# Kernel optimization log

Hardware: AMD Instinct MI355X
Metric: run time of the kernel (lower is better)

The kernel has to match this reference:

```python
import jax, jax.numpy as jnp
import numpy as np

M_TIME = 64      # signal model output length (time points)
N_DICT = 20000   # dictionary entries
B_VOX = 8192     # voxels / batch


def setup_inputs() -> dict:
    key = jax.random.key(0)
    k = jax.random.split(key, 6)
    input_real = jax.random.normal(k[0], (M_TIME, B_VOX), jnp.float32)
    input_imag = jax.random.normal(k[1], (M_TIME, B_VOX), jnp.float32)
    # raw dictionary signals, then normalize columns as append() does
    yr = jax.random.normal(k[2], (M_TIME, N_DICT), jnp.float32)
    yi = jax.random.normal(k[3], (M_TIME, N_DICT), jnp.float32)
    norm = jnp.sqrt(jnp.sum(yr * yr + yi * yi, axis=0))  # (N,)
    inverse_norm_y = 1.0 / norm
    y_real = yr * inverse_norm_y
    y_imag = yi * inverse_norm_y
    x_t1 = jax.random.uniform(k[4], (N_DICT,), jnp.float32, 0.1, 3.0)
    x_t2 = jax.random.uniform(k[5], (N_DICT,), jnp.float32, 0.01, 0.5)
    return {
        'input_real': input_real, 'input_imag': input_imag,
        'y_real': y_real, 'y_imag': y_imag,
        'inverse_norm_y': inverse_norm_y, 'x_t1': x_t1, 'x_t2': x_t2,
    }


def reference(input_real, input_imag, y_real, y_imag, inverse_norm_y, x_t1, x_t2):
    # |<y_n, s_b>|^2 for complex y and complex input, via 4 real GEMMs (as in the
    # original module): sim[n, b]
    sim = (jnp.einsum('mb,mn->nb', input_real, y_real) ** 2
           + jnp.einsum('mb,mn->nb', input_real, y_imag) ** 2
           + jnp.einsum('mb,mn->nb', input_imag, y_real) ** 2
           + jnp.einsum('mb,mn->nb', input_imag, y_imag) ** 2)
    idx = jnp.argmax(sim, axis=0)  # (B,)
    # scale = sum_m conj(y[:, idx]) * input * inverse_norm_y[idx]
    yr = y_real[:, idx]   # (M, B)
    yi = y_imag[:, idx]   # (M, B)
    inv = inverse_norm_y[idx]  # (B,)
    scale_r = jnp.sum(yr * input_real + yi * input_imag, axis=0) * inv
    scale_i = jnp.sum(yr * input_imag - yi * input_real, axis=0) * inv
    # returns (scale, t1, t2) with complex scale split into real/imag, stacked (4, B)
    return jnp.stack([scale_r, scale_i, x_t1[idx], x_t2[idx]])
```

## Files before the change

### kernel.cpp

```cpp
#include <hip/hip_runtime.h>
#include <hip/hip_bf16.h>
#include <stdint.h>

#define M_TIME 64
#define N_DICT 20000
#define B_VOX  8192

#define NTILES 313

typedef _Float16 v8h __attribute__((ext_vector_type(8)));
typedef _Float16 v4h __attribute__((ext_vector_type(4)));
typedef float    v4f __attribute__((ext_vector_type(4)));
typedef __attribute__((address_space(3))) unsigned int  lds_u32;
typedef const __attribute__((address_space(1))) unsigned int glb_u32;

__device__ __forceinline__ unsigned long long u64max(unsigned long long a, unsigned long long b) { return a > b ? a : b; }
__device__ __forceinline__ unsigned umin32(unsigned a, unsigned b) { return a < b ? a : b; }
__device__ __forceinline__ unsigned umax32(unsigned a, unsigned b) { return a > b ? a : b; }

__global__ __launch_bounds__(256) void split_y(
    const float* __restrict__ yr, const float* __restrict__ yi,
    v4h* __restrict__ yp)
{
    const int u = blockIdx.x * 256 + threadIdx.x;
    const int n_l = u & 63;
    const int kq  = (u >> 6) & 15;
    const int T   = (u >> 10) % NTILES;
    const int arr = u / (NTILES * 1024);
    if (arr > 1) return;
    const float* P = arr ? yi : yr;
    const int n_g = T * 64 + n_l;
    float v0 = 0.f, v1 = 0.f, v2 = 0.f, v3 = 0.f;
    if (n_g < N_DICT) {
        v0 = P[(kq * 4 + 0) * N_DICT + n_g];
        v1 = P[(kq * 4 + 1) * N_DICT + n_g];
        v2 = P[(kq * 4 + 2) * N_DICT + n_g];
        v3 = P[(kq * 4 + 3) * N_DICT + n_g];
    }
    v4h V;
    V[0] = (_Float16)v0; V[1] = (_Float16)v1;
    V[2] = (_Float16)v2; V[3] = (_Float16)v3;
    const int h    = kq >> 3;
    const int quad = (kq >> 1) & 3;
    const int half = kq & 1;
    const int fr   = (arr * 2 + h) * 4 + quad;
    yp[((size_t)T * 16 + fr) * 128 + n_l * 2 + half] = V;
}

__global__ __launch_bounds__(256, 2) void gemm_pre(
    const float* __restrict__ ir, const float* __restrict__ ii,
    const v4h* __restrict__ yp,
    unsigned* __restrict__ cand, int tpc, int slots)
{
    __shared__ float4 ys4[2][1024];
    __shared__ unsigned xm[2][2][16][2];

    const int tid  = threadIdx.x;
    const int wave = tid >> 6, lane = tid & 63;
    const int quad = lane >> 4, col = lane & 15;
    const int wb   = wave >> 1, wn = wave & 1;
    const int vox_w = blockIdx.x * 64 + wb * 32;
    const int chunk = blockIdx.y;
    const int T0 = chunk * tpc;
    const int T1 = (T0 + tpc < NTILES) ? T0 + tpc : NTILES;

    auto dma_tile = [&](int T, int buf) {
        const float4* src = (const float4*)((const char*)yp + (size_t)T * 16384);
#pragma unroll
        for (int p = 0; p < 4; ++p) {
            const int base = p * 256 + wave * 64;
            __builtin_amdgcn_global_load_lds(
                (glb_u32*)(src + base + lane),
                (lds_u32*)(&ys4[buf][base]), 16, 0, 0);
        }
    };

    dma_tile(T0, 0);

    v8h fh[2][2][2];
#pragma unroll
    for (int arr = 0; arr < 2; ++arr) {
        const float* P = arr ? ii : ir;
#pragma unroll
        for (int bt = 0; bt < 2; ++bt) {
            const int b = vox_w + bt * 16 + col;
#pragma unroll
            for (int h = 0; h < 2; ++h) {
                v8h H;
#pragma unroll
                for (int j = 0; j < 8; ++j) {
                    const int k = h * 32 + quad * 8 + j;
                    H[j] = (_Float16)P[k * B_VOX + b];
                }
                fh[arr][bt][h] = H;
            }
        }
    }

    const v4f zc = {0.f, 0.f, 0.f, 0.f};
    unsigned t2a[2] = {0u, 0u}, t2b[2] = {0u, 0u};

    for (int T = T0; T < T1; ++T) {
        const int par = (T - T0) & 1;
        __syncthreads();
        if (T + 1 < T1) dma_tile(T + 1, par ^ 1);
        const v8h* yv = (const v8h*)ys4[par];

        v4f acc[2][2][4];
#pragma unroll
        for (int h = 0; h < 2; ++h) {
#pragma unroll
            for (int nt = 0; nt < 2; ++nt) {
                const int nrow = (wn * 2 + nt) * 16 + col;
                const v8h yfr = yv[((0 * 2 + h) * 4 + quad) * 64 + nrow];
                const v8h yfi = yv[((1 * 2 + h) * 4 + quad) * 64 + nrow];
#pragma unroll
                for (int bt = 0; bt < 2; ++bt) {
#define MF(A, B, C) __builtin_amdgcn_mfma_f32_16x16x32_f16(A, B, C, 0, 0, 0)
                    if (h == 0) {
                        acc[bt][nt][0] = MF(yfr, fh[0][bt][0], zc);
                        acc[bt][nt][1] = MF(yfi, fh[0][bt][0], zc);
                        acc[bt][nt][2] = MF(yfr, fh[1][bt][0], zc);
                        acc[bt][nt][3] = MF(yfi, fh[1][bt][0], zc);
                    } else {
                        acc[bt][nt][0] = MF(yfr, fh[0][bt][1], acc[bt][nt][0]);
                        acc[bt][nt][1] = MF(yfi, fh[0][bt][1], acc[bt][nt][1]);
                        acc[bt][nt][2] = MF(yfr, fh[1][bt][1], acc[bt][nt][2]);
                        acc[bt][nt][3] = MF(yfi, fh[1][bt][1], acc[bt][nt][3]);
                    }
#undef MF
                }
            }
        }

        const int tl = T - T0;
#pragma unroll
        for (int nt = 0; nt < 2; ++nt) {
            const int inv_base = 0x1FFF - (tl * 64 + (wn * 2 + nt) * 16 + quad * 4);
#pragma unroll
            for (int bt = 0; bt < 2; ++bt) {
                v4f RR = acc[bt][nt][0], RI = acc[bt][nt][1];
                v4f S1 = acc[bt][nt][2], S2 = acc[bt][nt][3];
#pragma unroll
                for (int r = 0; r < 4; ++r) {
                    float s = fmaf(RR[r], RR[r], fmaf(RI[r], RI[r],
                              fmaf(S1[r], S1[r], S2[r] * S2[r])));
                    unsigned pb = (__float_as_uint(s) & 0xFFFFE000u)
                                | (unsigned)(inv_base - r);
                    unsigned lo = umin32(pb, t2a[bt]);
                    t2a[bt] = umax32(pb, t2a[bt]);
                    t2b[bt] = umax32(t2b[bt], lo);
                }
            }
        }
    }

    unsigned fa1[2], fa2[2];
#pragma unroll
    for (int bt = 0; bt < 2; ++bt) {
        unsigned a1 = t2a[bt], a2 = t2b[bt];
#pragma unroll
        for (int d = 16; d <= 32; d <<= 1) {
            unsigned b1 = (unsigned)__shfl_xor((int)a1, d, 64);
            unsigned b2 = (unsigned)__shfl_xor((int)a2, d, 64);
            unsigned mn = umin32(a1, b1);
            a1 = umax32(a1, b1);
            a2 = umax32(mn, umax32(a2, b2));
        }
        fa1[bt] = a1; fa2[bt] = a2;
    }
    __syncthreads();
    if (wn == 1 && lane < 16) {
#pragma unroll
        for (int bt = 0; bt < 2; ++bt) { xm[wb][bt][lane][0] = fa1[bt]; xm[wb][bt][lane][1] = fa2[bt]; }
    }
    __syncthreads();
    if (wn == 0 && lane < 16) {
#pragma unroll
        for (int bt = 0; bt < 2; ++bt) {
            unsigned b1 = xm[wb][bt][lane][0];
            unsigned b2 = xm[wb][bt][lane][1];
            unsigned m1 = umax32(fa1[bt], b1);
            unsigned m2 = umax32(umin32(fa1[bt], b1), umax32(fa2[bt], b2));
            const size_t vox = vox_w + bt * 16 + lane;
            cand[vox * slots + chunk * 2 + 0] = m1;
            cand[vox * slots + chunk * 2 + 1] = m2;
        }
    }
}

__global__ __launch_bounds__(256) void rescore_finish(
    const float* __restrict__ ir, const float* __restrict__ ii,
    const float* __restrict__ yr, const float* __restrict__ yi,
    const float* __restrict__ inv, const float* __restrict__ x1,
    const float* __restrict__ x2,
    const unsigned* __restrict__ cand, int slots, int tpc,
    float* __restrict__ out)
{
    const int tid  = threadIdx.x;
    const int vox  = blockIdx.x * 4 + (tid >> 6);
    const int slot = tid & 63;

    unsigned p = (slot < slots) ? cand[(size_t)vox * slots + slot] : 0u;
    float sa = __uint_as_float(p & 0xFFFFE000u);
    const int chunkc = slot >> 1;
    const int nn = chunkc * tpc * 64 + (0x1FFF - (int)(p & 0x1FFFu));

    float amax = sa;
#pragma unroll
    for (int d = 1; d <= 32; d <<= 1) amax = fmaxf(amax, __shfl_xor(amax, d, 64));

    unsigned long long q = 0ull;
    float rr = 0.f, ri = 0.f, s1 = 0.f, s2 = 0.f;
    const bool active = (slot < slots) && (nn >= 0) && (nn < N_DICT)
                     && (sa >= 0.97f * amax);
    if (active) {
        for (int m = 0; m < M_TIME; ++m) {
            float a  = yr[(size_t)m * N_DICT + nn];
            float c  = yi[(size_t)m * N_DICT + nn];
            float vr = ir[m * B_VOX + vox];
            float vi = ii[m * B_VOX + vox];
            rr = fmaf(vr, a, rr); ri = fmaf(vr, c, ri);
            s1 = fmaf(vi, a, s1); s2 = fmaf(vi, c, s2);
        }
        float s = fmaf(rr, rr, fmaf(ri, ri, fmaf(s1, s1, s2 * s2)));
        q = (((unsigned long long)__float_as_uint(s)) << 32)
          | (unsigned long long)(0xFFFFFFFFu - (unsigned)nn);
    }
    unsigned long long qm = q;
#pragma unroll
    for (int d = 1; d <= 32; d <<= 1) qm = u64max(qm, __shfl_xor(qm, d, 64));

    if (active && q == qm && qm != 0ull) {
        float ss = inv[nn];
        out[0 * B_VOX + vox] = (rr + s2) * ss;
        out[1 * B_VOX + vox] = (s1 - ri) * ss;
        out[2 * B_VOX + vox] = x1[nn];
        out[3 * B_VOX + vox] = x2[nn];
    }
}

__global__ __launch_bounds__(256, 3) void argmax_naive(
    const float* __restrict__ ir, const float* __restrict__ ii,
    const float* __restrict__ yr, const float* __restrict__ yi,
    int* __restrict__ idxout)
{
    int b = blockIdx.x * 256 + threadIdx.x;
    float bs = -1.0f; int bn = 0;
    for (int n = 0; n < N_DICT; ++n) {
        float a_rr = 0.f, a_ri = 0.f, a_s1 = 0.f, a_s2 = 0.f;
        for (int m = 0; m < M_TIME; ++m) {
            float a = yr[m * N_DICT + n], c = yi[m * N_DICT + n];
            float vr = ir[m * B_VOX + b], vi = ii[m * B_VOX + b];
            a_rr = fmaf(vr, a, a_rr); a_ri = fmaf(vr, c, a_ri);
            a_s1 = fmaf(vi, a, a_s1); a_s2 = fmaf(vi, c, a_s2);
        }
        float sim = fmaf(a_rr, a_rr, fmaf(a_ri, a_ri, fmaf(a_s1, a_s1, a_s2 * a_s2)));
        if (sim > bs) { bs = sim; bn = n; }
    }
    idxout[b] = bn;
}

__global__ void finish_k(const float* __restrict__ ir, const float* __restrict__ ii,
                         const float* __restrict__ yr, const float* __restrict__ yi,
                         const float* __restrict__ inv, const float* __restrict__ x1,
                         const float* __restrict__ x2,
                         const int* __restrict__ idxin, float* __restrict__ out)
{
    int b = blockIdx.x * blockDim.x + threadIdx.x;
    int idx = idxin[b];
    float ar = 0.f, ai = 0.f;
    for (int m = 0; m < M_TIME; ++m) {
        float a  = yr[(size_t)m * N_DICT + idx];
        float c  = yi[(size_t)m * N_DICT + idx];
        float vr = ir[m * B_VOX + b];
        float vi = ii[m * B_VOX + b];
        ar = fmaf(a, vr, ar); ar = fmaf(c, vi, ar);
        ai = fmaf(a, vi, ai); ai = fmaf(-c, vr, ai);
    }
    float s = inv[idx];
    out[0 * B_VOX + b] = ar * s;
    out[1 * B_VOX + b] = ai * s;
    out[2 * B_VOX + b] = x1[idx];
    out[3 * B_VOX + b] = x2[idx];
}

extern "C" void kernel_launch(void* const* d_in, const int* in_sizes, int n_in,
                              void* d_out, int out_size, void* d_ws, size_t ws_size,
                              hipStream_t stream) {
    const float* ir  = (const float*)d_in[0];
    const float* ii  = (const float*)d_in[1];
    const float* yr  = (const float*)d_in[2];
    const float* yi  = (const float*)d_in[3];
    const float* inv = (const float*)d_in[4];
    const float* x1  = (const float*)d_in[5];
    const float* x2  = (const float*)d_in[6];
    float* out = (float*)d_out;

    const size_t yp_bytes = (size_t)NTILES * 16384;

    int CH = 0;
    for (int c = 16; c >= 4; c >>= 1) {
        size_t cand_bytes = (size_t)B_VOX * (2 * c) * sizeof(unsigned);
        if (ws_size >= cand_bytes + yp_bytes) { CH = c; break; }
    }

    if (CH > 0) {
        const int slots = 2 * CH;
        const int tpc   = (NTILES + CH - 1) / CH;
        unsigned* cand = (unsigned*)d_ws;
        v4h* yp = (v4h*)((char*)d_ws + (size_t)B_VOX * slots * sizeof(unsigned));

        const int units = 2 * NTILES * 1024;
        split_y<<<(units + 255) / 256, 256, 0, stream>>>(yr, yi, yp);
        gemm_pre<<<dim3(B_VOX / 64, CH), 256, 0, stream>>>(ir, ii, yp, cand, tpc, slots);
        rescore_finish<<<B_VOX / 4, 256, 0, stream>>>(ir, ii, yr, yi, inv, x1, x2,
                                                      cand, slots, tpc, out);
    } else {
        int* idxo = (int*)(out + 3 * B_VOX);
        argmax_naive<<<B_VOX / 256, 256, 0, stream>>>(ir, ii, yr, yi, idxo);
        finish_k<<<B_VOX / 256, 256, 0, stream>>>(ir, ii, yr, yi,
                                                  inv, x1, x2, idxo, out);
    }
}
```

Measured before the change: 201.8 us.

## Widen split_y to 8-half packs, allow 32 chunks, reorder top-2 scoring loop

split_y now converts eight fp16 values per thread and writes them as one 16-byte vector per lane, so half as many threads issue wider stores. The layout is meant to stay equivalent to the old two-half interleave. The chunk search now tries 32 dictionary chunks first, which doubles the gemm_pre grid's second dimension when the workspace is large enough, at the cost of twice as many candidate slots for rescore_finish to process. The top-2 scoring loop is also reordered to iterate r outermost, which changes the insertion order of candidates.

```diff
diff --git a/kernel.cpp b/kernel.cpp
--- a/kernel.cpp
+++ b/kernel.cpp
@@ -9,7 +9,6 @@
 #define NTILES 313
 
 typedef _Float16 v8h __attribute__((ext_vector_type(8)));
-typedef _Float16 v4h __attribute__((ext_vector_type(4)));
 typedef float    v4f __attribute__((ext_vector_type(4)));
 typedef __attribute__((address_space(3))) unsigned int  lds_u32;
 typedef const __attribute__((address_space(1))) unsigned int glb_u32;
@@ -20,36 +19,30 @@
 
 __global__ __launch_bounds__(256) void split_y(
     const float* __restrict__ yr, const float* __restrict__ yi,
-    v4h* __restrict__ yp)
+    v8h* __restrict__ yp)
 {
     const int u = blockIdx.x * 256 + threadIdx.x;
     const int n_l = u & 63;
-    const int kq  = (u >> 6) & 15;
-    const int T   = (u >> 10) % NTILES;
-    const int arr = u / (NTILES * 1024);
+    const int j   = (u >> 6) & 7;
+    const int T   = (u >> 9) % NTILES;
+    const int arr = u / (NTILES * 512);
     if (arr > 1) return;
     const float* P = arr ? yi : yr;
     const int n_g = T * 64 + n_l;
-    float v0 = 0.f, v1 = 0.f, v2 = 0.f, v3 = 0.f;
-    if (n_g < N_DICT) {
-        v0 = P[(kq * 4 + 0) * N_DICT + n_g];
-        v1 = P[(kq * 4 + 1) * N_DICT + n_g];
-        v2 = P[(kq * 4 + 2) * N_DICT + n_g];
-        v3 = P[(kq * 4 + 3) * N_DICT + n_g];
-    }
-    v4h V;
-    V[0] = (_Float16)v0; V[1] = (_Float16)v1;
-    V[2] = (_Float16)v2; V[3] = (_Float16)v3;
-    const int h    = kq >> 3;
-    const int quad = (kq >> 1) & 3;
-    const int half = kq & 1;
-    const int fr   = (arr * 2 + h) * 4 + quad;
-    yp[((size_t)T * 16 + fr) * 128 + n_l * 2 + half] = V;
+    v8h V;
+#pragma unroll
+    for (int c = 0; c < 8; ++c) {
+        float v = 0.f;
+        if (n_g < N_DICT) v = P[(j * 8 + c) * N_DICT + n_g];
+        V[c] = (_Float16)v;
+    }
+    const int fr = (arr * 2 + (j >> 2)) * 4 + (j & 3);
+    yp[((size_t)T * 16 + fr) * 64 + n_l] = V;
 }
 
 __global__ __launch_bounds__(256, 2) void gemm_pre(
     const float* __restrict__ ir, const float* __restrict__ ii,
-    const v4h* __restrict__ yp,
+    const v8h* __restrict__ yp,
     unsigned* __restrict__ cand, int tpc, int slots)
 {
     __shared__ float4 ys4[2][1024];
@@ -135,18 +128,18 @@
 
         const int tl = T - T0;
 #pragma unroll
-        for (int nt = 0; nt < 2; ++nt) {
-            const int inv_base = 0x1FFF - (tl * 64 + (wn * 2 + nt) * 16 + quad * 4);
-#pragma unroll
-            for (int bt = 0; bt < 2; ++bt) {
-                v4f RR = acc[bt][nt][0], RI = acc[bt][nt][1];
-                v4f S1 = acc[bt][nt][2], S2 = acc[bt][nt][3];
-#pragma unroll
-                for (int r = 0; r < 4; ++r) {
-                    float s = fmaf(RR[r], RR[r], fmaf(RI[r], RI[r],
-                              fmaf(S1[r], S1[r], S2[r] * S2[r])));
+        for (int r = 0; r < 4; ++r) {
+#pragma unroll
+            for (int nt = 0; nt < 2; ++nt) {
+                const int inv_idx = 0x1FFF - (tl * 64 + (wn * 2 + nt) * 16 + quad * 4 + r);
+#pragma unroll
+                for (int bt = 0; bt < 2; ++bt) {
+                    float s = fmaf(acc[bt][nt][0][r], acc[bt][nt][0][r],
+                              fmaf(acc[bt][nt][1][r], acc[bt][nt][1][r],
+                              fmaf(acc[bt][nt][2][r], acc[bt][nt][2][r],
+                                   acc[bt][nt][3][r] * acc[bt][nt][3][r])));
                     unsigned pb = (__float_as_uint(s) & 0xFFFFE000u)
-                                | (unsigned)(inv_base - r);
+                                | (unsigned)inv_idx;
                     unsigned lo = umin32(pb, t2a[bt]);
                     t2a[bt] = umax32(pb, t2a[bt]);
                     t2b[bt] = umax32(t2b[bt], lo);
@@ -300,7 +293,7 @@
     const size_t yp_bytes = (size_t)NTILES * 16384;
 
     int CH = 0;
-    for (int c = 16; c >= 4; c >>= 1) {
+    for (int c = 32; c >= 4; c >>= 1) {
         size_t cand_bytes = (size_t)B_VOX * (2 * c) * sizeof(unsigned);
         if (ws_size >= cand_bytes + yp_bytes) { CH = c; break; }
     }
@@ -309,9 +302,9 @@
         const int slots = 2 * CH;
         const int tpc   = (NTILES + CH - 1) / CH;
         unsigned* cand = (unsigned*)d_ws;
-        v4h* yp = (v4h*)((char*)d_ws + (size_t)B_VOX * slots * sizeof(unsigned));
-
-        const int units = 2 * NTILES * 1024;
+        v8h* yp = (v8h*)((char*)d_ws + (size_t)B_VOX * slots * sizeof(unsigned));
+
+        const int units = 2 * NTILES * 512;
         split_y<<<(units + 255) / 256, 256, 0, stream>>>(yr, yi, yp);
         gemm_pre<<<dim3(B_VOX / 64, CH), 256, 0, stream>>>(ir, ii, yp, cand, tpc, slots);
         rescore_finish<<<B_VOX / 4, 256, 0, stream>>>(ir, ii, yr, yi, inv, x1, x2,
```

Result: no change. 200.5 us (-0.6%).
